# Kernel optimization log

Hardware: AMD Instinct MI355X
Metric: run time of the kernel (lower is better)

Reference implementation:

```python
import jax, jax.numpy as jnp
import numpy as np

B, L_Q, L_K = 16, 256, 256
Q_DIM, K_DIM, H_DIM, V_DIM = 256, 256, 128, 128


def setup_inputs() -> dict:
    key = jax.random.key(0)
    k1, k2, k3, k4, k5, k6 = jax.random.split(key, 6)
    query = jax.random.normal(k1, (B, L_Q, Q_DIM), dtype=jnp.float32)
    key_t = jax.random.normal(k2, (B, L_K, K_DIM), dtype=jnp.float32)
    value = jax.random.normal(k3, (B, L_Q, V_DIM), dtype=jnp.float32)
    # Linear weights stored as [in, out] for x @ W (equivalent to torch Linear, no bias)
    Wq = jax.random.normal(k4, (Q_DIM, H_DIM), dtype=jnp.float32) / np.sqrt(Q_DIM)
    Wk = jax.random.normal(k5, (K_DIM, H_DIM), dtype=jnp.float32) / np.sqrt(K_DIM)
    v = jax.random.uniform(k6, (H_DIM,), dtype=jnp.float32, minval=-0.1, maxval=0.1)
    return {"query": query, "key": key_t, "value": value, "Wq": Wq, "Wk": Wk, "v": v}


def reference(query, key, value, Wq, Wk, v):
    # Project first (equivalent to applying Linear after the expand, but cheaper):
    qp = jnp.einsum("bqd,dh->bqh", query, Wq)  # [B, l_q, h]
    kp = jnp.einsum("bkd,dh->bkh", key, Wk)    # [B, l_k, h]
    # score[b, k, q] = tanh(qp[b,q] + kp[b,k]) . v  -> [B, l_k, l_q]
    score = jnp.einsum("bkqh,h->bkq", jnp.tanh(qp[:, None, :, :] + kp[:, :, None, :]), v)
    attention = jax.nn.softmax(score, axis=-1)  # softmax over query positions (dim -1)
    context = jnp.einsum("bkq,bqv->bkv", attention, value)  # bmm
    return context, attention
```

## Files before the change

kernel.cpp:

```cpp
#include <hip/hip_runtime.h>

#define B_  16
#define LQ  256
#define LK  256
#define QD  256
#define HD  128
#define VD  128

#define SCALE2 2.8853900817779268f
#define L2E    1.4426950408889634f
#define CTX_SIZE (B_ * LK * VD)

typedef float v2f __attribute__((ext_vector_type(2)));

__device__ __forceinline__ float fast_exp2(float x) { return __builtin_amdgcn_exp2f(x); }
__device__ __forceinline__ float fast_rcp(float x)  { return __builtin_amdgcn_rcpf(x); }

__global__ __launch_bounds__(256) void proj_kernel(const float* __restrict__ query,
                                                   const float* __restrict__ key,
                                                   const float* __restrict__ Wq,
                                                   const float* __restrict__ Wk,
                                                   float* __restrict__ qe_t,
                                                   float* __restrict__ ke)
{
    __shared__ float  Xs[8][260];
    __shared__ float4 part[4][8][32];

    const int t = threadIdx.x;
    const bool isQ = (blockIdx.x < 512);
    const int blk  = isQ ? blockIdx.x : (blockIdx.x - 512);
    const int rows0 = blk * 8;
    const float* X = isQ ? query : key;
    const float* W = isQ ? Wq : Wk;

    {
        const int r = t >> 5;
        const int c = (t & 31) * 8;
        const float4 x0 = *(const float4*)(X + (size_t)(rows0 + r) * QD + c);
        const float4 x1 = *(const float4*)(X + (size_t)(rows0 + r) * QD + c + 4);
        *(float4*)&Xs[r][c]     = x0;
        *(float4*)&Xs[r][c + 4] = x1;
    }
    __syncthreads();

    const int w    = t >> 6;
    const int lane = t & 63;
    const int hg   = lane & 31;
    const int mb   = lane >> 5;

    float4 acc[4];
#pragma unroll
    for (int i = 0; i < 4; i++) acc[i] = make_float4(0.f, 0.f, 0.f, 0.f);

    const int kbase = w * 64;
#pragma unroll 4
    for (int kk = 0; kk < 64; kk++) {
        const int k = kbase + kk;
        const float4 wv = *(const float4*)(W + (size_t)k * HD + hg * 4);
#pragma unroll
        for (int mi = 0; mi < 4; mi++) {
            const float xv = Xs[mb + mi * 2][k];
            acc[mi].x += xv * wv.x;
            acc[mi].y += xv * wv.y;
            acc[mi].z += xv * wv.z;
            acc[mi].w += xv * wv.w;
        }
    }
#pragma unroll
    for (int mi = 0; mi < 4; mi++) part[w][mb + mi * 2][hg] = acc[mi];
    __syncthreads();

    {
        const int m   = t >> 5;
        const int hg2 = t & 31;
        float4 s = part[0][m][hg2];
        const float4 p1 = part[1][m][hg2];
        const float4 p2 = part[2][m][hg2];
        const float4 p3 = part[3][m][hg2];
        s.x += p1.x + p2.x + p3.x;
        s.y += p1.y + p2.y + p3.y;
        s.z += p1.z + p2.z + p3.z;
        s.w += p1.w + p2.w + p3.w;
        float4 e = make_float4(fast_exp2(s.x * SCALE2), fast_exp2(s.y * SCALE2),
                               fast_exp2(s.z * SCALE2), fast_exp2(s.w * SCALE2));
        const int row = rows0 + m;
        if (isQ) {
            const int b = row >> 8, q = row & 255;
            float* base = qe_t + ((size_t)b * HD + hg2 * 4) * LQ + q;
            base[0 * LQ] = e.x;
            base[1 * LQ] = e.y;
            base[2 * LQ] = e.z;
            base[3 * LQ] = e.w;
        } else {
            *(float4*)(ke + (size_t)row * HD + hg2 * 4) = e;
        }
    }
}

__global__ __launch_bounds__(256) void attn_kernel(const float* __restrict__ qe_t,
                                                   const float* __restrict__ ke,
                                                   const float* __restrict__ v,
                                                   const float* __restrict__ value,
                                                   float* __restrict__ out)
{
    __shared__ float  score_s[4][260];
    __shared__ float  attn_T[256][4];
    __shared__ float2 partc[4][4][64];

    const int t  = threadIdx.x;
    const int b  = blockIdx.x >> 6;
    const int k0 = (blockIdx.x & 63) << 2;

    const float* qeb = qe_t + (size_t)b * HD * LQ;
    const float* keb = ke + ((size_t)b * LK + k0) * HD;

    v2f acc[4];
#pragma unroll
    for (int i = 0; i < 4; i++) acc[i] = (v2f)0.f;

    const int q = t;
#pragma unroll 2
    for (int h0 = 0; h0 < HD; h0 += 8) {
        float qv[8];
#pragma unroll
        for (int j = 0; j < 8; j++) qv[j] = qeb[(size_t)(h0 + j) * LQ + q];
#pragma unroll
        for (int jp = 0; jp < 4; jp++) {
            v2f q2; q2.x = qv[2 * jp]; q2.y = qv[2 * jp + 1];
            const v2f vh2 = *(const v2f*)(v + h0 + 2 * jp);
#pragma unroll
            for (int kk = 0; kk < 4; kk++) {
                const v2f ke2 = *(const v2f*)(keb + kk * HD + h0 + 2 * jp);
                v2f tt = __builtin_elementwise_fma(q2, ke2, (v2f)1.0f);
                v2f r; r.x = fast_rcp(tt.x); r.y = fast_rcp(tt.y);
                acc[kk] = __builtin_elementwise_fma(vh2, r, acc[kk]);
            }
        }
    }
    float sumv = 0.f;
#pragma unroll
    for (int h = 0; h < HD; h++) sumv += v[h];

#pragma unroll
    for (int kk = 0; kk < 4; kk++)
        score_s[kk][q] = sumv - 2.f * (acc[kk].x + acc[kk].y);
    __syncthreads();

    const int w = t >> 6, lane = t & 63;
    {
        float x0 = score_s[w][lane];
        float x1 = score_s[w][lane + 64];
        float x2 = score_s[w][lane + 128];
        float x3 = score_s[w][lane + 192];
        float m = fmaxf(fmaxf(x0, x1), fmaxf(x2, x3));
#pragma unroll
        for (int off = 32; off >= 1; off >>= 1) m = fmaxf(m, __shfl_xor(m, off));
        float e0 = fast_exp2((x0 - m) * L2E);
        float e1 = fast_exp2((x1 - m) * L2E);
        float e2 = fast_exp2((x2 - m) * L2E);
        float e3 = fast_exp2((x3 - m) * L2E);
        float s = e0 + e1 + e2 + e3;
#pragma unroll
        for (int off = 32; off >= 1; off >>= 1) s += __shfl_xor(s, off);
        const float rs = fast_rcp(s);
        e0 *= rs; e1 *= rs; e2 *= rs; e3 *= rs;
        attn_T[lane][w]       = e0;
        attn_T[lane + 64][w]  = e1;
        attn_T[lane + 128][w] = e2;
        attn_T[lane + 192][w] = e3;
        float* ao = out + CTX_SIZE + ((size_t)(b * LK + k0 + w)) * LQ;
        ao[lane]       = e0;
        ao[lane + 64]  = e1;
        ao[lane + 128] = e2;
        ao[lane + 192] = e3;
    }
    __syncthreads();

    {
        const int vd2 = lane * 2;
        const float* valb = value + (size_t)b * LQ * VD;
        v2f c0 = (v2f)0.f, c1 = (v2f)0.f, c2 = (v2f)0.f, c3 = (v2f)0.f;
#pragma unroll 4
        for (int i = 0; i < 64; i++) {
            const int q2 = (w << 6) + i;
            const float4 a = *(const float4*)&attn_T[q2][0];
            const v2f vv = *(const v2f*)(valb + (size_t)q2 * VD + vd2);
            c0 = __builtin_elementwise_fma((v2f)(a.x), vv, c0);
            c1 = __builtin_elementwise_fma((v2f)(a.y), vv, c1);
            c2 = __builtin_elementwise_fma((v2f)(a.z), vv, c2);
            c3 = __builtin_elementwise_fma((v2f)(a.w), vv, c3);
        }
        partc[w][0][lane] = *(const float2*)&c0;
        partc[w][1][lane] = *(const float2*)&c1;
        partc[w][2][lane] = *(const float2*)&c2;
        partc[w][3][lane] = *(const float2*)&c3;
    }
    __syncthreads();
    {
        const int kg = t >> 6, l2 = t & 63;
        const float2 p0 = partc[0][kg][l2];
        const float2 p1 = partc[1][kg][l2];
        const float2 p2 = partc[2][kg][l2];
        const float2 p3 = partc[3][kg][l2];
        float2 s;
        s.x = p0.x + p1.x + p2.x + p3.x;
        s.y = p0.y + p1.y + p2.y + p3.y;
        *(float2*)(out + ((size_t)(b * LK + k0 + kg)) * VD + l2 * 2) = s;
    }
}

extern "C" void kernel_launch(void* const* d_in, const int* in_sizes, int n_in,
                              void* d_out, int out_size, void* d_ws, size_t ws_size,
                              hipStream_t stream)
{
    const float* query = (const float*)d_in[0];
    const float* key   = (const float*)d_in[1];
    const float* value = (const float*)d_in[2];
    const float* Wq    = (const float*)d_in[3];
    const float* Wk    = (const float*)d_in[4];
    const float* v     = (const float*)d_in[5];
    float* out = (float*)d_out;

    float* qe_t = (float*)d_ws;
    float* kew  = qe_t + (size_t)B_ * HD * LQ;

    proj_kernel<<<dim3(1024), 256, 0, stream>>>(query, key, Wq, Wk, qe_t, kew);
    attn_kernel<<<dim3(1024), 256, 0, stream>>>(qe_t, kew, v, value, out);
}
```

Baseline: 104.5 us.

## Split attention score reduction over hidden dim across two thread halves

Doubles the attention block to 512 threads. Each half of the block computes partial tanh-scores over 64 of the 128 hidden units, and the halves are combined in shared memory before the softmax. The context bmm is also split across 8 waves of 32 query rows each, with an 8-way partial-sum reduction. This adds parallelism and latency hiding to the rcp-bound score loop, at the cost of extra shared memory, idle waves during the softmax, and a larger reduction.

Measured after the change: 136.3 us. +30.5%, slower.

```diff
diff --git a/kernel.cpp b/kernel.cpp
--- a/kernel.cpp
+++ b/kernel.cpp
@@ -97,15 +97,15 @@
     }
 }
 
-__global__ __launch_bounds__(256) void attn_kernel(const float* __restrict__ qe_t,
-                                                   const float* __restrict__ ke,
-                                                   const float* __restrict__ v,
-                                                   const float* __restrict__ value,
-                                                   float* __restrict__ out)
+__global__ __launch_bounds__(512, 8) void attn_kernel(const float* __restrict__ qe_t,
+                                                      const float* __restrict__ ke,
+                                                      const float* __restrict__ v,
+                                                      const float* __restrict__ value,
+                                                      float* __restrict__ out)
 {
-    __shared__ float  score_s[4][260];
+    __shared__ float  score_s[2][4][258];
     __shared__ float  attn_T[256][4];
-    __shared__ float2 partc[4][4][64];
+    __shared__ float2 partc[8][4][64];
 
     const int t  = threadIdx.x;
     const int b  = blockIdx.x >> 6;
@@ -114,44 +114,47 @@
     const float* qeb = qe_t + (size_t)b * HD * LQ;
     const float* keb = ke + ((size_t)b * LK + k0) * HD;
 
+    const int q     = t & 255;
+    const int hbase = (t >> 8) * 64;
+
     v2f acc[4];
 #pragma unroll
     for (int i = 0; i < 4; i++) acc[i] = (v2f)0.f;
 
-    const int q = t;
 #pragma unroll 2
-    for (int h0 = 0; h0 < HD; h0 += 8) {
+    for (int h0 = 0; h0 < 64; h0 += 8) {
+        const int hA = hbase + h0;
         float qv[8];
 #pragma unroll
-        for (int j = 0; j < 8; j++) qv[j] = qeb[(size_t)(h0 + j) * LQ + q];
+        for (int j = 0; j < 8; j++) qv[j] = qeb[(size_t)(hA + j) * LQ + q];
 #pragma unroll
         for (int jp = 0; jp < 4; jp++) {
             v2f q2; q2.x = qv[2 * jp]; q2.y = qv[2 * jp + 1];
-            const v2f vh2 = *(const v2f*)(v + h0 + 2 * jp);
+            const v2f vh2 = *(const v2f*)(v + hA + 2 * jp);
 #pragma unroll
             for (int kk = 0; kk < 4; kk++) {
-                const v2f ke2 = *(const v2f*)(keb + kk * HD + h0 + 2 * jp);
+                const v2f ke2 = *(const v2f*)(keb + kk * HD + hA + 2 * jp);
                 v2f tt = __builtin_elementwise_fma(q2, ke2, (v2f)1.0f);
                 v2f r; r.x = fast_rcp(tt.x); r.y = fast_rcp(tt.y);
                 acc[kk] = __builtin_elementwise_fma(vh2, r, acc[kk]);
             }
         }
     }
-    float sumv = 0.f;
-#pragma unroll
-    for (int h = 0; h < HD; h++) sumv += v[h];
-
+    const int hh = t >> 8;
 #pragma unroll
     for (int kk = 0; kk < 4; kk++)
-        score_s[kk][q] = sumv - 2.f * (acc[kk].x + acc[kk].y);
+        score_s[hh][kk][q] = acc[kk].x + acc[kk].y;
     __syncthreads();
 
     const int w = t >> 6, lane = t & 63;
-    {
-        float x0 = score_s[w][lane];
-        float x1 = score_s[w][lane + 64];
-        float x2 = score_s[w][lane + 128];
-        float x3 = score_s[w][lane + 192];
+    if (w < 4) {
+        float sumv = 0.f;
+#pragma unroll
+        for (int h = 0; h < HD; h++) sumv += v[h];
+        float x0 = sumv - 2.f * (score_s[0][w][lane]       + score_s[1][w][lane]);
+        float x1 = sumv - 2.f * (score_s[0][w][lane + 64]  + score_s[1][w][lane + 64]);
+        float x2 = sumv - 2.f * (score_s[0][w][lane + 128] + score_s[1][w][lane + 128]);
+        float x3 = sumv - 2.f * (score_s[0][w][lane + 192] + score_s[1][w][lane + 192]);
         float m = fmaxf(fmaxf(x0, x1), fmaxf(x2, x3));
 #pragma unroll
         for (int off = 32; off >= 1; off >>= 1) m = fmaxf(m, __shfl_xor(m, off));
@@ -181,8 +184,8 @@
         const float* valb = value + (size_t)b * LQ * VD;
         v2f c0 = (v2f)0.f, c1 = (v2f)0.f, c2 = (v2f)0.f, c3 = (v2f)0.f;
 #pragma unroll 4
-        for (int i = 0; i < 64; i++) {
-            const int q2 = (w << 6) + i;
+        for (int i = 0; i < 32; i++) {
+            const int q2 = (w << 5) + i;
             const float4 a = *(const float4*)&attn_T[q2][0];
             const v2f vv = *(const v2f*)(valb + (size_t)q2 * VD + vd2);
             c0 = __builtin_elementwise_fma((v2f)(a.x), vv, c0);
@@ -196,15 +199,15 @@
         partc[w][3][lane] = *(const float2*)&c3;
     }
     __syncthreads();
-    {
+    if (t < 256) {
         const int kg = t >> 6, l2 = t & 63;
-        const float2 p0 = partc[0][kg][l2];
-        const float2 p1 = partc[1][kg][l2];
-        const float2 p2 = partc[2][kg][l2];
-        const float2 p3 = partc[3][kg][l2];
-        float2 s;
-        s.x = p0.x + p1.x + p2.x + p3.x;
-        s.y = p0.y + p1.y + p2.y + p3.y;
+        float2 s = partc[0][kg][l2];
+#pragma unroll
+        for (int p = 1; p < 8; p++) {
+            const float2 pp = partc[p][kg][l2];
+            s.x += pp.x;
+            s.y += pp.y;
+        }
         *(float2*)(out + ((size_t)(b * LK + k0 + kg)) * VD + l2 * 2) = s;
     }
 }
@@ -225,5 +228,5 @@
     float* kew  = qe_t + (size_t)B_ * HD * LQ;
 
     proj_kernel<<<dim3(1024), 256, 0, stream>>>(query, key, Wq, Wk, qe_t, kew);
-    attn_kernel<<<dim3(1024), 256, 0, stream>>>(qe_t, kew, v, value, out);
+    attn_kernel<<<dim3(1024), 512, 0, stream>>>(qe_t, kew, v, value, out);
 }
```

## Halve keys per block, double grid, and interleave qe in float4 groups

Applied to the files above, without the earlier changes.

The attention kernel now handles 2 key rows per block instead of 4, which doubles the grid to 2048 blocks and adds a launch-bounds occupancy hint. The q-side projection output is relaid out as [b][h/4][q][4], so each thread reads one float4 per four hidden dims instead of strided scalars. This is meant to raise occupancy and make the exp/rcp score loop use vectorized loads. In exchange, each qe value is reused across fewer keys, so qe and value traffic per key doubles, and some waves sit idle during the softmax and reduction phases.

Result: no change. 106.0 us (+1.5%).

```diff
diff --git a/kernel.cpp b/kernel.cpp
--- a/kernel.cpp
+++ b/kernel.cpp
@@ -86,68 +86,71 @@
         const int row = rows0 + m;
         if (isQ) {
             const int b = row >> 8, q = row & 255;
-            float* base = qe_t + ((size_t)b * HD + hg2 * 4) * LQ + q;
-            base[0 * LQ] = e.x;
-            base[1 * LQ] = e.y;
-            base[2 * LQ] = e.z;
-            base[3 * LQ] = e.w;
+            *(float4*)(qe_t + ((size_t)(b * 32 + hg2) * 256 + q) * 4) = e;
         } else {
             *(float4*)(ke + (size_t)row * HD + hg2 * 4) = e;
         }
     }
 }
 
-__global__ __launch_bounds__(256) void attn_kernel(const float* __restrict__ qe_t,
-                                                   const float* __restrict__ ke,
-                                                   const float* __restrict__ v,
-                                                   const float* __restrict__ value,
-                                                   float* __restrict__ out)
+__global__ __launch_bounds__(256, 8) void attn_kernel(const float* __restrict__ qe_t,
+                                                      const float* __restrict__ ke,
+                                                      const float* __restrict__ v,
+                                                      const float* __restrict__ value,
+                                                      float* __restrict__ out)
 {
-    __shared__ float  score_s[4][260];
-    __shared__ float  attn_T[256][4];
-    __shared__ float2 partc[4][4][64];
+    __shared__ float  score_s[2][260];
+    __shared__ float  attn_T[256][2];
+    __shared__ float2 partc[4][2][64];
 
     const int t  = threadIdx.x;
-    const int b  = blockIdx.x >> 6;
-    const int k0 = (blockIdx.x & 63) << 2;
-
-    const float* qeb = qe_t + (size_t)b * HD * LQ;
-    const float* keb = ke + ((size_t)b * LK + k0) * HD;
-
-    v2f acc[4];
-#pragma unroll
-    for (int i = 0; i < 4; i++) acc[i] = (v2f)0.f;
-
+    const int b  = blockIdx.x >> 7;
+    const int k0 = (blockIdx.x & 127) << 1;
+
+    const float* qeb = qe_t + (size_t)b * (32 * 256 * 4);
+    const float* kep = ke + ((size_t)b * LK + k0) * HD;
+
+    v2f acc0 = (v2f)0.f, acc1 = (v2f)0.f;
     const int q = t;
-#pragma unroll 2
-    for (int h0 = 0; h0 < HD; h0 += 8) {
-        float qv[8];
-#pragma unroll
-        for (int j = 0; j < 8; j++) qv[j] = qeb[(size_t)(h0 + j) * LQ + q];
-#pragma unroll
-        for (int jp = 0; jp < 4; jp++) {
-            v2f q2; q2.x = qv[2 * jp]; q2.y = qv[2 * jp + 1];
-            const v2f vh2 = *(const v2f*)(v + h0 + 2 * jp);
-#pragma unroll
-            for (int kk = 0; kk < 4; kk++) {
-                const v2f ke2 = *(const v2f*)(keb + kk * HD + h0 + 2 * jp);
-                v2f tt = __builtin_elementwise_fma(q2, ke2, (v2f)1.0f);
-                v2f r; r.x = fast_rcp(tt.x); r.y = fast_rcp(tt.y);
-                acc[kk] = __builtin_elementwise_fma(vh2, r, acc[kk]);
-            }
+#pragma unroll 4
+    for (int g = 0; g < 32; g++) {
+        const float4 qv4 = *(const float4*)(qeb + ((size_t)g * 256 + q) * 4);
+        const int hA = g * 4;
+        const v2f vha = *(const v2f*)(v + hA);
+        const v2f vhb = *(const v2f*)(v + hA + 2);
+        v2f q2a; q2a.x = qv4.x; q2a.y = qv4.y;
+        v2f q2b; q2b.x = qv4.z; q2b.y = qv4.w;
+        {
+            const v2f ka = *(const v2f*)(kep + hA);
+            const v2f kb = *(const v2f*)(kep + hA + 2);
+            v2f ta = __builtin_elementwise_fma(q2a, ka, (v2f)1.0f);
+            v2f ra; ra.x = fast_rcp(ta.x); ra.y = fast_rcp(ta.y);
+            acc0 = __builtin_elementwise_fma(vha, ra, acc0);
+            v2f tb = __builtin_elementwise_fma(q2b, kb, (v2f)1.0f);
+            v2f rb; rb.x = fast_rcp(tb.x); rb.y = fast_rcp(tb.y);
+            acc0 = __builtin_elementwise_fma(vhb, rb, acc0);
+        }
+        {
+            const v2f ka = *(const v2f*)(kep + HD + hA);
+            const v2f kb = *(const v2f*)(kep + HD + hA + 2);
+            v2f ta = __builtin_elementwise_fma(q2a, ka, (v2f)1.0f);
+            v2f ra; ra.x = fast_rcp(ta.x); ra.y = fast_rcp(ta.y);
+            acc1 = __builtin_elementwise_fma(vha, ra, acc1);
+            v2f tb = __builtin_elementwise_fma(q2b, kb, (v2f)1.0f);
+            v2f rb; rb.x = fast_rcp(tb.x); rb.y = fast_rcp(tb.y);
+            acc1 = __builtin_elementwise_fma(vhb, rb, acc1);
         }
     }
     float sumv = 0.f;
 #pragma unroll
     for (int h = 0; h < HD; h++) sumv += v[h];
 
-#pragma unroll
-    for (int kk = 0; kk < 4; kk++)
-        score_s[kk][q] = sumv - 2.f * (acc[kk].x + acc[kk].y);
+    score_s[0][q] = sumv - 2.f * (acc0.x + acc0.y);
+    score_s[1][q] = sumv - 2.f * (acc1.x + acc1.y);
     __syncthreads();
 
     const int w = t >> 6, lane = t & 63;
-    {
+    if (w < 2) {
         float x0 = score_s[w][lane];
         float x1 = score_s[w][lane + 64];
         float x2 = score_s[w][lane + 128];
@@ -179,24 +182,20 @@
     {
         const int vd2 = lane * 2;
         const float* valb = value + (size_t)b * LQ * VD;
-        v2f c0 = (v2f)0.f, c1 = (v2f)0.f, c2 = (v2f)0.f, c3 = (v2f)0.f;
+        v2f c0 = (v2f)0.f, c1 = (v2f)0.f;
 #pragma unroll 4
         for (int i = 0; i < 64; i++) {
             const int q2 = (w << 6) + i;
-            const float4 a = *(const float4*)&attn_T[q2][0];
+            const float2 a = *(const float2*)&attn_T[q2][0];
             const v2f vv = *(const v2f*)(valb + (size_t)q2 * VD + vd2);
             c0 = __builtin_elementwise_fma((v2f)(a.x), vv, c0);
             c1 = __builtin_elementwise_fma((v2f)(a.y), vv, c1);
-            c2 = __builtin_elementwise_fma((v2f)(a.z), vv, c2);
-            c3 = __builtin_elementwise_fma((v2f)(a.w), vv, c3);
         }
         partc[w][0][lane] = *(const float2*)&c0;
         partc[w][1][lane] = *(const float2*)&c1;
-        partc[w][2][lane] = *(const float2*)&c2;
-        partc[w][3][lane] = *(const float2*)&c3;
-    }
-    __syncthreads();
-    {
+    }
+    __syncthreads();
+    if (t < 128) {
         const int kg = t >> 6, l2 = t & 63;
         const float2 p0 = partc[0][kg][l2];
         const float2 p1 = partc[1][kg][l2];
@@ -225,5 +224,5 @@
     float* kew  = qe_t + (size_t)B_ * HD * LQ;
 
     proj_kernel<<<dim3(1024), 256, 0, stream>>>(query, key, Wq, Wk, qe_t, kew);
-    attn_kernel<<<dim3(1024), 256, 0, stream>>>(qe_t, kew, v, value, out);
+    attn_kernel<<<dim3(2048), 256, 0, stream>>>(qe_t, kew, v, value, out);
 }
```

## Pair reciprocals in tanh score loop and interleave qe layout for float4 loads

Applied to the files above, without the earlier changes.

The hot score loop now shares one reciprocal between two key rows (1/(t0*t1), then scaled by the other factor), which halves the rcp transcendental count per element. The constant sum(v) and the factor -2 are folded into the softmax by taking the min of the raw accumulator and scaling the exponent by 2*log2(e), since the offset cancels in softmax. The qe projection output is stored as interleaved groups of four h values per q, so the attention kernel reads it with float4 loads instead of scalar strided loads. The paired product of two (1+qe*ke) terms could overflow or lose precision for large exponentials.

New measurement: 101.9 us. -2.5%, faster.

```diff
diff --git a/kernel.cpp b/kernel.cpp
--- a/kernel.cpp
+++ b/kernel.cpp
@@ -8,7 +8,6 @@
 #define VD  128
 
 #define SCALE2 2.8853900817779268f
-#define L2E    1.4426950408889634f
 #define CTX_SIZE (B_ * LK * VD)
 
 typedef float v2f __attribute__((ext_vector_type(2)));
@@ -86,11 +85,7 @@
         const int row = rows0 + m;
         if (isQ) {
             const int b = row >> 8, q = row & 255;
-            float* base = qe_t + ((size_t)b * HD + hg2 * 4) * LQ + q;
-            base[0 * LQ] = e.x;
-            base[1 * LQ] = e.y;
-            base[2 * LQ] = e.z;
-            base[3 * LQ] = e.w;
+            *(float4*)(qe_t + ((size_t)(b * 32 + hg2) * 256 + q) * 4) = e;
         } else {
             *(float4*)(ke + (size_t)row * HD + hg2 * 4) = e;
         }
@@ -111,39 +106,46 @@
     const int b  = blockIdx.x >> 6;
     const int k0 = (blockIdx.x & 63) << 2;
 
-    const float* qeb = qe_t + (size_t)b * HD * LQ;
-    const float* keb = ke + ((size_t)b * LK + k0) * HD;
-
-    v2f acc[4];
-#pragma unroll
-    for (int i = 0; i < 4; i++) acc[i] = (v2f)0.f;
-
+    const float* qeb = qe_t + (size_t)b * (32 * 256 * 4);
+    const float* kep = ke + ((size_t)b * LK + k0) * HD;
+
+    float acc0 = 0.f, acc1 = 0.f, acc2 = 0.f, acc3 = 0.f;
     const int q = t;
-#pragma unroll 2
-    for (int h0 = 0; h0 < HD; h0 += 8) {
-        float qv[8];
-#pragma unroll
-        for (int j = 0; j < 8; j++) qv[j] = qeb[(size_t)(h0 + j) * LQ + q];
-#pragma unroll
-        for (int jp = 0; jp < 4; jp++) {
-            v2f q2; q2.x = qv[2 * jp]; q2.y = qv[2 * jp + 1];
-            const v2f vh2 = *(const v2f*)(v + h0 + 2 * jp);
-#pragma unroll
-            for (int kk = 0; kk < 4; kk++) {
-                const v2f ke2 = *(const v2f*)(keb + kk * HD + h0 + 2 * jp);
-                v2f tt = __builtin_elementwise_fma(q2, ke2, (v2f)1.0f);
-                v2f r; r.x = fast_rcp(tt.x); r.y = fast_rcp(tt.y);
-                acc[kk] = __builtin_elementwise_fma(vh2, r, acc[kk]);
-            }
-        }
-    }
-    float sumv = 0.f;
-#pragma unroll
-    for (int h = 0; h < HD; h++) sumv += v[h];
-
-#pragma unroll
-    for (int kk = 0; kk < 4; kk++)
-        score_s[kk][q] = sumv - 2.f * (acc[kk].x + acc[kk].y);
+
+#define PAIR_STEP(QJ, VJ, KA, KB, KC, KD)                          \
+    {                                                              \
+        const float t0 = fmaf(QJ, KA, 1.0f);                       \
+        const float t1 = fmaf(QJ, KB, 1.0f);                       \
+        const float t2 = fmaf(QJ, KC, 1.0f);                       \
+        const float t3 = fmaf(QJ, KD, 1.0f);                       \
+        const float r01 = fast_rcp(t0 * t1);                       \
+        const float r23 = fast_rcp(t2 * t3);                       \
+        acc0 = fmaf(VJ * t1, r01, acc0);                           \
+        acc1 = fmaf(VJ * t0, r01, acc1);                           \
+        acc2 = fmaf(VJ * t3, r23, acc2);                           \
+        acc3 = fmaf(VJ * t2, r23, acc3);                           \
+    }
+
+#pragma unroll 4
+    for (int g = 0; g < 32; g++) {
+        const float4 qv = *(const float4*)(qeb + ((size_t)g * 256 + q) * 4);
+        const int hA = g * 4;
+        const float4 va = *(const float4*)(v + hA);
+        const float4 ka = *(const float4*)(kep + hA);
+        const float4 kb = *(const float4*)(kep + HD + hA);
+        const float4 kc = *(const float4*)(kep + 2 * HD + hA);
+        const float4 kd = *(const float4*)(kep + 3 * HD + hA);
+        PAIR_STEP(qv.x, va.x, ka.x, kb.x, kc.x, kd.x)
+        PAIR_STEP(qv.y, va.y, ka.y, kb.y, kc.y, kd.y)
+        PAIR_STEP(qv.z, va.z, ka.z, kb.z, kc.z, kd.z)
+        PAIR_STEP(qv.w, va.w, ka.w, kb.w, kc.w, kd.w)
+    }
+#undef PAIR_STEP
+
+    score_s[0][q] = acc0;
+    score_s[1][q] = acc1;
+    score_s[2][q] = acc2;
+    score_s[3][q] = acc3;
     __syncthreads();
 
     const int w = t >> 6, lane = t & 63;
@@ -152,13 +154,13 @@
         float x1 = score_s[w][lane + 64];
         float x2 = score_s[w][lane + 128];
         float x3 = score_s[w][lane + 192];
-        float m = fmaxf(fmaxf(x0, x1), fmaxf(x2, x3));
-#pragma unroll
-        for (int off = 32; off >= 1; off >>= 1) m = fmaxf(m, __shfl_xor(m, off));
-        float e0 = fast_exp2((x0 - m) * L2E);
-        float e1 = fast_exp2((x1 - m) * L2E);
-        float e2 = fast_exp2((x2 - m) * L2E);
-        float e3 = fast_exp2((x3 - m) * L2E);
+        float m = fminf(fminf(x0, x1), fminf(x2, x3));
+#pragma unroll
+        for (int off = 32; off >= 1; off >>= 1) m = fminf(m, __shfl_xor(m, off));
+        float e0 = fast_exp2((m - x0) * SCALE2);
+        float e1 = fast_exp2((m - x1) * SCALE2);
+        float e2 = fast_exp2((m - x2) * SCALE2);
+        float e3 = fast_exp2((m - x3) * SCALE2);
         float s = e0 + e1 + e2 + e3;
 #pragma unroll
         for (int off = 32; off >= 1; off >>= 1) s += __shfl_xor(s, off);
```
